# Optimization experiments

Hardware: AMD Instinct MI355X
Metric: run time of the kernel (lower is better)

Reference implementation:

```python
import jax, jax.numpy as jnp
import numpy as np
from jax.scipy.stats import norm

H, W = 512, 512
HP, WP = 3, 3            # plane window
T_BINS, R_BINS = 180, 360  # accumulator dims (theta, rho)
THR_VAR = 100.0
ORIGIN = (0, 0)


def setup_inputs() -> dict:
    key = jax.random.key(0)
    k1, _ = jax.random.split(key)
    img = jax.random.uniform(k1, (H, W), dtype=jnp.float32)
    mask = jnp.ones((H, W), dtype=jnp.float32)
    return {"img": img, "mask": mask}


def _shift(img, dx, dy):
    # edge-clamped shifted view, matches xi = clip(hi+dx, 0, H-1)
    ri = jnp.clip(jnp.arange(H) + dx, 0, H - 1)
    ci = jnp.clip(jnp.arange(W) + dy, 0, W - 1)
    return img[ri][:, ci]


def reference(img, mask):
    img = img.astype(jnp.float32)
    dxs = range(-(HP // 2), HP // 2 + 1)
    dys = range(-(WP // 2), WP // 2 + 1)
    sum_x2 = float(sum(dx * dx for dx in dxs) * WP)  # = 6 for 3x3
    sum_y2 = float(sum(dy * dy for dy in dys) * HP)
    n_win = float(HP * WP)

    # ---- local plane fit (vectorized over all pixels, loop over 9 offsets) ----
    alpha = jnp.zeros((H, W), jnp.float32)
    beta = jnp.zeros((H, W), jnp.float32)
    gamma = jnp.zeros((H, W), jnp.float32)
    for dx in dxs:
        for dy in dys:
            s = _shift(img, dx, dy)
            alpha = alpha + dx * s
            beta = beta + dy * s
            gamma = gamma + s
    alpha = alpha / sum_x2 + 1e-6
    beta = beta / sum_y2 + 1e-6
    gamma = gamma / n_win

    # ---- residual variance (faithful to source: uses img[xi, wi]) ----
    eps2 = jnp.zeros((H, W), jnp.float32)
    for dx in dxs:
        row_s = _shift(img, dx, 0)  # img[clip(hi+dx), wi]
        for dy in dys:
            r = row_s - alpha * dy - beta * dx - gamma
            eps2 = eps2 + r * r
    noise_var = eps2 / (n_win - 2.0)
    var_alpha = noise_var / sum_x2
    var_beta = noise_var / sum_y2
    covar_ab = jnp.zeros_like(noise_var)  # sum_xy == 0 for symmetric window

    # ---- polar coordinates + uncertainty propagation ----
    theta = jnp.arctan(beta / alpha)  # in (-pi/2, pi/2)
    xg = (jnp.arange(H, dtype=jnp.float32) - ORIGIN[0])[:, None]
    yg = (jnp.arange(W, dtype=jnp.float32) - ORIGIN[1])[None, :]
    ct, st = jnp.cos(theta), jnp.sin(theta)
    rho = xg * ct + yg * st
    g2 = (alpha * alpha + beta * beta)
    var_theta = (beta * beta * var_alpha + alpha * alpha * var_beta
                 - 2.0 * alpha * beta * covar_ab) / (g2 * g2)
    drho_dt = -xg * st + yg * ct
    var_rho = drho_dt * drho_dt * var_theta

    # ---- Gaussian soft-voting into the accumulator ----
    theta_min, theta_max = -np.pi / 2, np.pi / 2
    rho_max = float(np.sqrt(H ** 2 + W ** 2))
    rho_min = -rho_max
    t_bin = (theta_max - theta_min) / (T_BINS - 1)
    r_bin = (rho_max - rho_min) / (R_BINS - 1)
    # bin i covers [center - bin/2, center + bin/2]
    t_edges = theta_min + (jnp.arange(T_BINS + 1, dtype=jnp.float32) - 0.5) * t_bin
    r_edges = rho_min + (jnp.arange(R_BINS + 1, dtype=jnp.float32) - 0.5) * r_bin

    valid = ((var_theta <= THR_VAR) & (var_rho <= THR_VAR)).astype(jnp.float32) * mask

    P = H * W
    thf = theta.reshape(P)
    rhf = rho.reshape(P)
    sig_t = jnp.sqrt(var_theta + 1e-12).reshape(P)
    sig_r = jnp.sqrt(var_rho + 1e-12).reshape(P)
    vf = valid.reshape(P)

    # per-pixel probability mass in each theta / rho bin (marginal Gaussian CDFs)
    cdf_t = norm.cdf((t_edges[None, :] - thf[:, None]) / sig_t[:, None])  # (P, T+1)
    wt = (cdf_t[:, 1:] - cdf_t[:, :-1]) * vf[:, None]                    # (P, T)
    cdf_r = norm.cdf((r_edges[None, :] - rhf[:, None]) / sig_r[:, None])  # (P, R+1)
    wr = cdf_r[:, 1:] - cdf_r[:, :-1]                                     # (P, R)

    acc = jnp.einsum('pt,pr->tr', wt, wr)  # (T_BINS, R_BINS) accumulated votes
    return acc
```

## Files before the change

kernel.cpp:

```cpp
#include <hip/hip_runtime.h>
#include <math.h>

#define H 512
#define W 512
#define TBINS 180
#define RBINS 360
#define NPIX (H*W)
#define NCELL (TBINS*RBINS)

#define THETA_MIN (-1.5707963267948966f)
#define T_BIN ((float)(3.141592653589793 / 179.0))
#define R_MIN (-724.0773439350246f)
#define R_BIN ((float)(2.0 * 724.0773439350246 / 359.0))
#define THR_VAR 100.0f
#define WSIG 6.0f

#define NT 6
#define KB 80
#define BCAP 32768
#define MPAD 192
#define PADC 32

typedef short v8s __attribute__((ext_vector_type(8)));
typedef float v4f __attribute__((ext_vector_type(4)));

__device__ __forceinline__ float phi_cdf(float z) {
    return 0.5f * erfcf(-0.70710678118654752f * z);
}
__device__ __forceinline__ unsigned short f2bf(float f) {
    unsigned u = __float_as_uint(f);
    return (unsigned short)((u + 0x7FFF + ((u >> 16) & 1)) >> 16);
}
__device__ __forceinline__ float bf2f(unsigned short b) {
    return __uint_as_float(((unsigned)b) << 16);
}

__global__ void prep_kernel(const float* __restrict__ img,
                            const float* __restrict__ mask,
                            int* __restrict__ counts,
                            float4* __restrict__ recs,
                            float* __restrict__ mvs,
                            float* __restrict__ out) {
    __shared__ int lcnt[NT], gbase[NT];
    int tid = threadIdx.x;
    int gid = blockIdx.x * blockDim.x + tid;
    if (gid < NCELL) out[gid] = 0.0f;
    if (tid < NT) lcnt[tid] = 0;
    __syncthreads();

    int p = gid;
    int hi = p >> 9, wi = p & (W - 1);
    float mv = mask[p];

    int xm = max(hi - 1, 0), xp = min(hi + 1, H - 1);
    int ym = max(wi - 1, 0), yp = min(wi + 1, W - 1);
    const float* r0 = img + xm * W;
    const float* r1 = img + hi * W;
    const float* r2 = img + xp * W;
    float s00 = r0[ym], s01 = r0[wi], s02 = r0[yp];
    float s10 = r1[ym], s11 = r1[wi], s12 = r1[yp];
    float s20 = r2[ym], s21 = r2[wi], s22 = r2[yp];

    float alpha_s = (s20 + s21 + s22) - (s00 + s01 + s02);
    float beta_s  = (s02 + s12 + s22) - (s00 + s10 + s20);
    float gsum    = s00 + s01 + s02 + s10 + s11 + s12 + s20 + s21 + s22;

    float alpha = alpha_s * (1.0f / 6.0f) + 1e-6f;
    float beta  = beta_s  * (1.0f / 6.0f) + 1e-6f;
    float gamma = gsum * (1.0f / 9.0f);

    float cvals[3] = { s01, s11, s21 };
    float eps2 = 0.0f;
    #pragma unroll
    for (int ix = 0; ix < 3; ++ix) {
        float dx = (float)(ix - 1);
        float c = cvals[ix];
        #pragma unroll
        for (int iy = 0; iy < 3; ++iy) {
            float dy = (float)(iy - 1);
            float r = c - alpha * dy - beta * dx - gamma;
            eps2 += r * r;
        }
    }
    float noise_var = eps2 * (1.0f / 7.0f);
    float va = noise_var * (1.0f / 6.0f);
    float g2 = alpha * alpha + beta * beta;
    float var_theta = (beta * beta * va + alpha * alpha * va) / (g2 * g2);

    float x = (float)hi, y = (float)wi;
    float inv_g = rsqrtf(g2);
    float cta = fabsf(alpha) * inv_g;
    float sta = (alpha < 0.0f ? -beta : beta) * inv_g;
    float drho_a = -x * sta + y * cta;
    float var_rho_a = drho_a * drho_a * var_theta;
    bool maybe = (var_theta <= THR_VAR) && (var_rho_a <= THR_VAR * 1.01f) && (mv != 0.0f);

    int myNt[2] = { -1, -1 };
    int myPos[2];
    float4 rc;
    if (maybe) {
        float theta = atanf(beta / alpha);
        float ct = cosf(theta), st = sinf(theta);
        float rho = x * ct + y * st;
        float drho = -x * st + y * ct;
        float var_rho = drho * drho * var_theta;
        if (var_rho <= THR_VAR) {
            float sig_t = sqrtf(var_theta + 1e-12f);
            float sig_r = sqrtf(var_rho + 1e-12f);
            float radr = WSIG * sig_r;
            int rlo = max((int)floorf((rho - radr - R_MIN) / R_BIN - 0.5f), 0);
            int rhi = min((int)ceilf((rho + radr - R_MIN) / R_BIN + 0.5f), RBINS - 1);
            if (rhi >= rlo) {
                rc.x = theta; rc.y = 1.0f / sig_t; rc.z = rho; rc.w = 1.0f / sig_r;
                int nt0 = rlo >> 6, nt1 = rhi >> 6;
                for (int nt = nt0; nt <= nt1; ++nt) {
                    int k = nt - nt0;
                    myNt[k] = nt;
                    myPos[k] = atomicAdd(&lcnt[nt], 1);
                }
            }
        }
    }
    __syncthreads();
    if (tid < NT) {
        int c = lcnt[tid];
        gbase[tid] = c ? atomicAdd(&counts[tid * PADC], c) : 0;
    }
    __syncthreads();
    #pragma unroll
    for (int k = 0; k < 2; ++k) {
        if (myNt[k] >= 0) {
            int pos = gbase[myNt[k]] + myPos[k];
            if (pos < BCAP) {
                recs[myNt[k] * BCAP + pos] = rc;
                mvs[myNt[k] * BCAP + pos] = mv;
            }
        }
    }
}

__global__ void __launch_bounds__(512)
gemm_kernel(const float4* __restrict__ recs,
            const float* __restrict__ mvs,
            const int* __restrict__ counts,
            float* __restrict__ out) {
    __shared__ __align__(16) unsigned short Ah[MPAD * 32], Al[MPAD * 32];
    __shared__ __align__(16) unsigned short Bh[64 * 32],  Bl[64 * 32];
    __shared__ float4 prec[32];
    __shared__ float  pmv[32];

    int nt = blockIdx.x % NT, kb = blockIdx.x / NT;
    int tid = threadIdx.x;
    int lane = tid & 63, wv = tid >> 6;
    int nsub = wv & 3, mhalf = wv >> 2;
    int c0 = nt * 64;
    int nbmax = min(63, RBINS - 1 - c0);

    int cn = min(counts[nt * PADC], BCAP);
    int nck = (cn + 31) >> 5;
    if (kb >= nck) return;

    v4f zero = {0.f, 0.f, 0.f, 0.f};
    v4f acc[6];
    #pragma unroll
    for (int i = 0; i < 6; ++i) acc[i] = zero;

    const float4* rb = recs + (size_t)nt * BCAP;
    const float*  mb = mvs + (size_t)nt * BCAP;

    int pix = tid & 31, g = tid >> 5;

    for (int ck = kb; ck < nck; ck += KB) {
        int k0 = ck << 5;
        int k1 = min(k0 + 32, cn);
        if (ck != kb) __syncthreads();
        if (tid < 32) {
            int idx = k0 + tid;
            float4 rc; rc.x = 0.f; rc.y = 0.f; rc.z = 0.f; rc.w = 0.f;
            float m = 0.f;
            if (idx < k1) { rc = rb[idx]; m = mb[idx]; }
            prec[tid] = rc; pmv[tid] = m;
        }
        __syncthreads();

        float4 rc = prec[pix];
        float m = pmv[pix];
        float v[17];
        if (g < 12) {
            int e0 = g << 4;
            if (rc.y != 0.0f) {
                float sigt = 1.0f / rc.y;
                int wx = max((int)floorf((rc.x - WSIG * sigt - THETA_MIN) / T_BIN - 0.5f), 0);
                int wy = min((int)ceilf((rc.x + WSIG * sigt - THETA_MIN) / T_BIN + 0.5f), TBINS - 1);
                #pragma unroll
                for (int i = 0; i <= 16; ++i) {
                    int e = e0 + i;
                    float val;
                    if (e < wx) val = 0.0f;
                    else if (e > wy + 1) val = 1.0f;
                    else {
                        float edge = THETA_MIN + ((float)e - 0.5f) * T_BIN;
                        val = phi_cdf((edge - rc.x) * rc.y);
                    }
                    v[i] = val;
                }
            } else {
                #pragma unroll
                for (int i = 0; i <= 16; ++i) v[i] = 0.0f;
            }
            int sb = e0 * 32 + pix;
            #pragma unroll
            for (int i = 0; i < 16; ++i) {
                float wt = (v[i + 1] - v[i]) * m;
                unsigned short hb = f2bf(wt);
                Ah[sb + i * 32] = hb;
                Al[sb + i * 32] = f2bf(wt - bf2f(hb));
            }
        } else {
            int n0 = (g - 12) << 4;
            if (rc.y != 0.0f) {
                float sigr = 1.0f / rc.w;
                int wz = max((int)floorf((rc.z - WSIG * sigr - R_MIN) / R_BIN - 0.5f) - c0, 0);
                int ww = min((int)ceilf((rc.z + WSIG * sigr - R_MIN) / R_BIN + 0.5f) - c0, nbmax);
                #pragma unroll
                for (int i = 0; i <= 16; ++i) {
                    int n = n0 + i;
                    float val;
                    if (n < wz) val = 0.0f;
                    else if (n > ww + 1) val = 1.0f;
                    else {
                        float edge = R_MIN + ((float)(c0 + n) - 0.5f) * R_BIN;
                        val = phi_cdf((edge - rc.z) * rc.w);
                    }
                    v[i] = val;
                }
            } else {
                #pragma unroll
                for (int i = 0; i <= 16; ++i) v[i] = 0.0f;
            }
            int sb = n0 * 32 + pix;
            #pragma unroll
            for (int i = 0; i < 16; ++i) {
                float wr = v[i + 1] - v[i];
                unsigned short hb = f2bf(wr);
                Bh[sb + i * 32] = hb;
                Bl[sb + i * 32] = f2bf(wr - bf2f(hb));
            }
        }
        __syncthreads();

        int kq = (lane >> 4) * 8;
        int mr = lane & 15;
        v8s bh = *((__shared__ v8s*)&Bh[(nsub * 16 + mr) * 32 + kq]);
        v8s bl = *((__shared__ v8s*)&Bl[(nsub * 16 + mr) * 32 + kq]);
        #pragma unroll
        for (int mt = 0; mt < 6; ++mt) {
            int mbase = (mhalf * 6 + mt) * 16;
            v8s ah = *((__shared__ v8s*)&Ah[(mbase + mr) * 32 + kq]);
            v8s al = *((__shared__ v8s*)&Al[(mbase + mr) * 32 + kq]);
            acc[mt] = __builtin_amdgcn_mfma_f32_16x16x32_bf16(ah, bh, acc[mt], 0, 0, 0);
            acc[mt] = __builtin_amdgcn_mfma_f32_16x16x32_bf16(ah, bl, acc[mt], 0, 0, 0);
            acc[mt] = __builtin_amdgcn_mfma_f32_16x16x32_bf16(al, bh, acc[mt], 0, 0, 0);
        }
    }

    int gcol = c0 + nsub * 16 + (lane & 15);
    if (gcol < RBINS) {
        int rq = (lane >> 4) * 4;
        #pragma unroll
        for (int mt = 0; mt < 6; ++mt) {
            int rbase = (mhalf * 6 + mt) * 16 + rq;
            #pragma unroll
            for (int r = 0; r < 4; ++r) {
                int row = rbase + r;
                float v = acc[mt][r];
                if (row < TBINS && v != 0.0f)
                    atomicAdd(&out[row * RBINS + gcol], v);
            }
        }
    }
}

extern "C" void kernel_launch(void* const* d_in, const int* in_sizes, int n_in,
                              void* d_out, int out_size, void* d_ws, size_t ws_size,
                              hipStream_t stream) {
    const float* img  = (const float*)d_in[0];
    const float* mask = (const float*)d_in[1];
    float* out = (float*)d_out;

    char* ws = (char*)d_ws;
    int*    counts = (int*)ws;
    float4* recs   = (float4*)(ws + 1024);
    float*  mvs    = (float*)(ws + 1024 + (size_t)NT * BCAP * 16);

    hipMemsetAsync(counts, 0, NT * PADC * sizeof(int), stream);
    prep_kernel<<<NPIX / 256, 256, 0, stream>>>(img, mask, counts, recs, mvs, out);
    gemm_kernel<<<NT * KB, 512, 0, stream>>>(recs, mvs, counts, out);
}
```

Before: 93.23 us.

## Replace global atomic bucket compaction with per-block slots and in-kernel prefix scan

```diff
diff --git a/kernel.cpp b/kernel.cpp
--- a/kernel.cpp
+++ b/kernel.cpp
@@ -17,9 +17,9 @@
 
 #define NT 6
 #define KB 80
-#define BCAP 32768
+#define NBLK 1024
+#define SCAP 256
 #define MPAD 192
-#define PADC 32
 
 typedef short v8s __attribute__((ext_vector_type(8)));
 typedef float v4f __attribute__((ext_vector_type(4)));
@@ -37,13 +37,14 @@
 
 __global__ void prep_kernel(const float* __restrict__ img,
                             const float* __restrict__ mask,
-                            int* __restrict__ counts,
+                            int* __restrict__ cblk,
                             float4* __restrict__ recs,
                             float* __restrict__ mvs,
                             float* __restrict__ out) {
-    __shared__ int lcnt[NT], gbase[NT];
+    __shared__ int lcnt[NT];
     int tid = threadIdx.x;
-    int gid = blockIdx.x * blockDim.x + tid;
+    int b = blockIdx.x;
+    int gid = b * blockDim.x + tid;
     if (gid < NCELL) out[gid] = 0.0f;
     if (tid < NT) lcnt[tid] = 0;
     __syncthreads();
@@ -122,19 +123,13 @@
         }
     }
     __syncthreads();
-    if (tid < NT) {
-        int c = lcnt[tid];
-        gbase[tid] = c ? atomicAdd(&counts[tid * PADC], c) : 0;
-    }
-    __syncthreads();
+    if (tid < NT) cblk[tid * NBLK + b] = lcnt[tid];
     #pragma unroll
     for (int k = 0; k < 2; ++k) {
         if (myNt[k] >= 0) {
-            int pos = gbase[myNt[k]] + myPos[k];
-            if (pos < BCAP) {
-                recs[myNt[k] * BCAP + pos] = rc;
-                mvs[myNt[k] * BCAP + pos] = mv;
-            }
+            int idx = (myNt[k] * NBLK + b) * SCAP + myPos[k];
+            recs[idx] = rc;
+            mvs[idx]  = mv;
         }
     }
 }
@@ -142,12 +137,14 @@
 __global__ void __launch_bounds__(512)
 gemm_kernel(const float4* __restrict__ recs,
             const float* __restrict__ mvs,
-            const int* __restrict__ counts,
+            const int* __restrict__ cblk,
             float* __restrict__ out) {
     __shared__ __align__(16) unsigned short Ah[MPAD * 32], Al[MPAD * 32];
     __shared__ __align__(16) unsigned short Bh[64 * 32],  Bl[64 * 32];
     __shared__ float4 prec[32];
     __shared__ float  pmv[32];
+    __shared__ int    pref[NBLK];
+    __shared__ int    wsum[8], woff[8];
 
     int nt = blockIdx.x % NT, kb = blockIdx.x / NT;
     int tid = threadIdx.x;
@@ -156,7 +153,28 @@
     int c0 = nt * 64;
     int nbmax = min(63, RBINS - 1 - c0);
 
-    int cn = min(counts[nt * PADC], BCAP);
+    const int* cb = cblk + nt * NBLK;
+    int a0 = cb[2 * tid], a1 = cb[2 * tid + 1];
+    int s = a0 + a1;
+    #pragma unroll
+    for (int d = 1; d < 64; d <<= 1) {
+        int u = __shfl_up(s, d);
+        if (lane >= d) s += u;
+    }
+    if (lane == 63) wsum[wv] = s;
+    __syncthreads();
+    if (tid == 0) {
+        int r = 0;
+        #pragma unroll
+        for (int i = 0; i < 8; ++i) { woff[i] = r; r += wsum[i]; }
+    }
+    __syncthreads();
+    int base = woff[wv] + s;
+    pref[2 * tid]     = base - a1;
+    pref[2 * tid + 1] = base;
+    __syncthreads();
+
+    int cn = pref[NBLK - 1];
     int nck = (cn + 31) >> 5;
     if (kb >= nck) return;
 
@@ -165,8 +183,8 @@
     #pragma unroll
     for (int i = 0; i < 6; ++i) acc[i] = zero;
 
-    const float4* rb = recs + (size_t)nt * BCAP;
-    const float*  mb = mvs + (size_t)nt * BCAP;
+    const float4* rb = recs + (size_t)nt * NBLK * SCAP;
+    const float*  mb = mvs + (size_t)nt * NBLK * SCAP;
 
     int pix = tid & 31, g = tid >> 5;
 
@@ -175,10 +193,18 @@
         int k1 = min(k0 + 32, cn);
         if (ck != kb) __syncthreads();
         if (tid < 32) {
-            int idx = k0 + tid;
+            int r = k0 + tid;
             float4 rc; rc.x = 0.f; rc.y = 0.f; rc.z = 0.f; rc.w = 0.f;
             float m = 0.f;
-            if (idx < k1) { rc = rb[idx]; m = mb[idx]; }
+            if (r < k1) {
+                int pos = 0;
+                #pragma unroll
+                for (int st = 512; st >= 1; st >>= 1)
+                    if (pos + st <= NBLK && pref[pos + st - 1] <= r) pos += st;
+                int off = r - (pos ? pref[pos - 1] : 0);
+                int idx = pos * SCAP + off;
+                rc = rb[idx]; m = mb[idx];
+            }
             prec[tid] = rc; pmv[tid] = m;
         }
         __syncthreads();
@@ -289,11 +315,10 @@
     float* out = (float*)d_out;
 
     char* ws = (char*)d_ws;
-    int*    counts = (int*)ws;
-    float4* recs   = (float4*)(ws + 1024);
-    float*  mvs    = (float*)(ws + 1024 + (size_t)NT * BCAP * 16);
-
-    hipMemsetAsync(counts, 0, NT * PADC * sizeof(int), stream);
-    prep_kernel<<<NPIX / 256, 256, 0, stream>>>(img, mask, counts, recs, mvs, out);
-    gemm_kernel<<<NT * KB, 512, 0, stream>>>(recs, mvs, counts, out);
-}
+    int*    cblk = (int*)ws;
+    float4* recs = (float4*)(ws + 32768);
+    float*  mvs  = (float*)(ws + 32768 + (size_t)NT * NBLK * SCAP * 16);
+
+    prep_kernel<<<NPIX / 256, 256, 0, stream>>>(img, mask, cblk, recs, mvs, out);
+    gemm_kernel<<<NT * KB, 512, 0, stream>>>(recs, mvs, cblk, out);
+}
```

Measured after the change: 83.79 us. 1.11x faster.

## Replace atomic output accumulation with per-block partial slabs and a reduce kernel

Applied to the files above, without the earlier changes.

```diff
diff --git a/kernel.cpp b/kernel.cpp
--- a/kernel.cpp
+++ b/kernel.cpp
@@ -6,7 +6,6 @@
 #define TBINS 180
 #define RBINS 360
 #define NPIX (H*W)
-#define NCELL (TBINS*RBINS)
 
 #define THETA_MIN (-1.5707963267948966f)
 #define T_BIN ((float)(3.141592653589793 / 179.0))
@@ -16,10 +15,10 @@
 #define WSIG 6.0f
 
 #define NT 6
-#define KB 80
+#define KB 256
 #define BCAP 32768
+#define PADC 32
 #define MPAD 192
-#define PADC 32
 
 typedef short v8s __attribute__((ext_vector_type(8)));
 typedef float v4f __attribute__((ext_vector_type(4)));
@@ -39,12 +38,10 @@
                             const float* __restrict__ mask,
                             int* __restrict__ counts,
                             float4* __restrict__ recs,
-                            float* __restrict__ mvs,
-                            float* __restrict__ out) {
+                            float* __restrict__ mvs) {
     __shared__ int lcnt[NT], gbase[NT];
     int tid = threadIdx.x;
     int gid = blockIdx.x * blockDim.x + tid;
-    if (gid < NCELL) out[gid] = 0.0f;
     if (tid < NT) lcnt[tid] = 0;
     __syncthreads();
 
@@ -143,7 +140,8 @@
 gemm_kernel(const float4* __restrict__ recs,
             const float* __restrict__ mvs,
             const int* __restrict__ counts,
-            float* __restrict__ out) {
+            int* __restrict__ nw,
+            float* __restrict__ part) {
     __shared__ __align__(16) unsigned short Ah[MPAD * 32], Al[MPAD * 32];
     __shared__ __align__(16) unsigned short Bh[64 * 32],  Bl[64 * 32];
     __shared__ float4 prec[32];
@@ -158,6 +156,7 @@
 
     int cn = min(counts[nt * PADC], BCAP);
     int nck = (cn + 31) >> 5;
+    if (kb == 0 && tid == 0) nw[nt] = min(nck, KB);
     if (kb >= nck) return;
 
     v4f zero = {0.f, 0.f, 0.f, 0.f};
@@ -167,7 +166,6 @@
 
     const float4* rb = recs + (size_t)nt * BCAP;
     const float*  mb = mvs + (size_t)nt * BCAP;
-
     int pix = tid & 31, g = tid >> 5;
 
     for (int ck = kb; ck < nck; ck += KB) {
@@ -176,75 +174,67 @@
         if (ck != kb) __syncthreads();
         if (tid < 32) {
             int idx = k0 + tid;
-            float4 rc; rc.x = 0.f; rc.y = 0.f; rc.z = 0.f; rc.w = 0.f;
+            float4 rcv; rcv.x = 0.f; rcv.y = 0.f; rcv.z = 0.f; rcv.w = 0.f;
             float m = 0.f;
-            if (idx < k1) { rc = rb[idx]; m = mb[idx]; }
-            prec[tid] = rc; pmv[tid] = m;
+            if (idx < k1) { rcv = rb[idx]; m = mb[idx]; }
+            prec[tid] = rcv; pmv[tid] = m;
         }
         __syncthreads();
 
-        float4 rc = prec[pix];
-        float m = pmv[pix];
-        float v[17];
-        if (g < 12) {
-            int e0 = g << 4;
-            if (rc.y != 0.0f) {
+        {
+            float4 rc = prec[pix];
+            float m = pmv[pix];
+            bool live = (rc.y != 0.0f);
+            if (g < 12) {
+                int e0 = g << 4;
                 float sigt = 1.0f / rc.y;
                 int wx = max((int)floorf((rc.x - WSIG * sigt - THETA_MIN) / T_BIN - 0.5f), 0);
                 int wy = min((int)ceilf((rc.x + WSIG * sigt - THETA_MIN) / T_BIN + 0.5f), TBINS - 1);
-                #pragma unroll
+                int sb = e0 * 32 + pix;
+                float prev = 0.0f;
+                #pragma unroll 1
                 for (int i = 0; i <= 16; ++i) {
                     int e = e0 + i;
                     float val;
-                    if (e < wx) val = 0.0f;
+                    if (!live || e < wx) val = 0.0f;
                     else if (e > wy + 1) val = 1.0f;
                     else {
                         float edge = THETA_MIN + ((float)e - 0.5f) * T_BIN;
                         val = phi_cdf((edge - rc.x) * rc.y);
                     }
-                    v[i] = val;
+                    if (i > 0) {
+                        float wt = (val - prev) * m;
+                        unsigned short hb = f2bf(wt);
+                        Ah[sb + (i - 1) * 32] = hb;
+                        Al[sb + (i - 1) * 32] = f2bf(wt - bf2f(hb));
+                    }
+                    prev = val;
                 }
             } else {
-                #pragma unroll
-                for (int i = 0; i <= 16; ++i) v[i] = 0.0f;
-            }
-            int sb = e0 * 32 + pix;
-            #pragma unroll
-            for (int i = 0; i < 16; ++i) {
-                float wt = (v[i + 1] - v[i]) * m;
-                unsigned short hb = f2bf(wt);
-                Ah[sb + i * 32] = hb;
-                Al[sb + i * 32] = f2bf(wt - bf2f(hb));
-            }
-        } else {
-            int n0 = (g - 12) << 4;
-            if (rc.y != 0.0f) {
+                int n0 = (g - 12) << 4;
                 float sigr = 1.0f / rc.w;
                 int wz = max((int)floorf((rc.z - WSIG * sigr - R_MIN) / R_BIN - 0.5f) - c0, 0);
                 int ww = min((int)ceilf((rc.z + WSIG * sigr - R_MIN) / R_BIN + 0.5f) - c0, nbmax);
-                #pragma unroll
+                int sb = n0 * 32 + pix;
+                float prev = 0.0f;
+                #pragma unroll 1
                 for (int i = 0; i <= 16; ++i) {
                     int n = n0 + i;
                     float val;
-                    if (n < wz) val = 0.0f;
+                    if (!live || n < wz) val = 0.0f;
                     else if (n > ww + 1) val = 1.0f;
                     else {
                         float edge = R_MIN + ((float)(c0 + n) - 0.5f) * R_BIN;
                         val = phi_cdf((edge - rc.z) * rc.w);
                     }
-                    v[i] = val;
+                    if (i > 0) {
+                        float wr = val - prev;
+                        unsigned short hb = f2bf(wr);
+                        Bh[sb + (i - 1) * 32] = hb;
+                        Bl[sb + (i - 1) * 32] = f2bf(wr - bf2f(hb));
+                    }
+                    prev = val;
                 }
-            } else {
-                #pragma unroll
-                for (int i = 0; i <= 16; ++i) v[i] = 0.0f;
-            }
-            int sb = n0 * 32 + pix;
-            #pragma unroll
-            for (int i = 0; i < 16; ++i) {
-                float wr = v[i + 1] - v[i];
-                unsigned short hb = f2bf(wr);
-                Bh[sb + i * 32] = hb;
-                Bl[sb + i * 32] = f2bf(wr - bf2f(hb));
             }
         }
         __syncthreads();
@@ -264,20 +254,49 @@
         }
     }
 
-    int gcol = c0 + nsub * 16 + (lane & 15);
-    if (gcol < RBINS) {
-        int rq = (lane >> 4) * 4;
+    float* slab = part + (size_t)(nt * KB + kb) * (MPAD * 64);
+    int col = nsub * 16 + (lane & 15);
+    int rq = (lane >> 4) * 4;
+    #pragma unroll
+    for (int mt = 0; mt < 6; ++mt) {
+        int rbase = (mhalf * 6 + mt) * 16 + rq;
         #pragma unroll
-        for (int mt = 0; mt < 6; ++mt) {
-            int rbase = (mhalf * 6 + mt) * 16 + rq;
-            #pragma unroll
-            for (int r = 0; r < 4; ++r) {
-                int row = rbase + r;
-                float v = acc[mt][r];
-                if (row < TBINS && v != 0.0f)
-                    atomicAdd(&out[row * RBINS + gcol], v);
-            }
-        }
+        for (int r = 0; r < 4; ++r)
+            slab[(rbase + r) * 64 + col] = acc[mt][r];
+    }
+}
+
+__global__ void __launch_bounds__(1024)
+reduce_kernel(const float4* __restrict__ part, const int* __restrict__ nw,
+              float4* __restrict__ out) {
+    __shared__ float4 sdata[1024];
+    int t = blockIdx.x / 45;
+    int tid = threadIdx.x;
+    int qi = tid & 63, jg = tid >> 6;
+    int q = (blockIdx.x % 45) * 64 + qi;
+    int n = nw[t];
+    const float4* p = part + (size_t)t * KB * (MPAD * 16) + q;
+    float4 s; s.x = 0.f; s.y = 0.f; s.z = 0.f; s.w = 0.f;
+    #pragma unroll 4
+    for (int j = jg; j < n; j += 16) {
+        float4 v = p[(size_t)j * (MPAD * 16)];
+        s.x += v.x; s.y += v.y; s.z += v.z; s.w += v.w;
+    }
+    sdata[tid] = s;
+    __syncthreads();
+    #pragma unroll
+    for (int h = 8; h >= 1; h >>= 1) {
+        if (jg < h) {
+            float4 o = sdata[(jg + h) * 64 + qi];
+            s.x += o.x; s.y += o.y; s.z += o.z; s.w += o.w;
+            sdata[tid] = s;
+        }
+        __syncthreads();
+    }
+    if (jg == 0) {
+        int row = q >> 4, c4 = q & 15;
+        if (!(t == 5 && c4 >= 10))
+            out[row * 90 + t * 16 + c4] = s;
     }
 }
 
@@ -289,11 +308,19 @@
     float* out = (float*)d_out;
 
     char* ws = (char*)d_ws;
+    size_t off_recs = 1024;
+    size_t off_mvs  = off_recs + (size_t)NT * BCAP * 16;
+    size_t off_nw   = off_mvs + (size_t)NT * BCAP * 4;
+    size_t off_part = off_nw + 1024;
+
     int*    counts = (int*)ws;
-    float4* recs   = (float4*)(ws + 1024);
-    float*  mvs    = (float*)(ws + 1024 + (size_t)NT * BCAP * 16);
+    float4* recs   = (float4*)(ws + off_recs);
+    float*  mvs    = (float*)(ws + off_mvs);
+    int*    nw     = (int*)(ws + off_nw);
+    float*  part   = (float*)(ws + off_part);
 
     hipMemsetAsync(counts, 0, NT * PADC * sizeof(int), stream);
-    prep_kernel<<<NPIX / 256, 256, 0, stream>>>(img, mask, counts, recs, mvs, out);
-    gemm_kernel<<<NT * KB, 512, 0, stream>>>(recs, mvs, counts, out);
-}
+    prep_kernel<<<NPIX / 256, 256, 0, stream>>>(img, mask, counts, recs, mvs);
+    gemm_kernel<<<NT * KB, 512, 0, stream>>>(recs, mvs, counts, nw, part);
+    reduce_kernel<<<270, 1024, 0, stream>>>((const float4*)part, nw, (float4*)out);
+}
```

Measured after the change: 87.11 us. 6.6% less time.
